# Kernel optimization log

Hardware: AMD Instinct MI355X
Metric: run time of the kernel (lower is better)

Reference implementation:

```python
import jax, jax.numpy as jnp
import numpy as np

B, C, H = 8, 768, 12
TH = TW = 16
SH = SW = 32
N = TH * TW + SH * SW  # 1280


def setup_inputs() -> dict:
    key = jax.random.key(0)
    k1, k2, k3 = jax.random.split(key, 3)
    return {
        "x": jax.random.normal(k1, (B, N, C), jnp.float32),
        "qkv_w": jax.random.normal(k2, (3 * C, C), jnp.float32) * 0.02,
        "proj_w": jax.random.normal(k3, (C, C), jnp.float32) * 0.02,
        "proj_b": jnp.zeros((C,), jnp.float32),
        "t_h": TH, "t_w": TW, "s_h": SH, "s_w": SW,
    }


def reference(x, qkv_w, proj_w, proj_b, t_h, t_w, s_h, s_w):
    Bb, Nn, Cc = x.shape
    hd = Cc // H
    scale = hd ** -0.5
    nt = t_h * t_w
    ns = s_h * s_w
    # qkv projection: torch Linear computes x @ W.T
    qkv = (x @ qkv_w.T).reshape(Bb, Nn, 3, H, hd).transpose(2, 0, 3, 1, 4)
    q, k, v = qkv[0], qkv[1], qkv[2]  # each [B, H, N, hd]
    q_mt, q_s = q[:, :, :nt], q[:, :, nt:]
    k_mt, v_mt = k[:, :, :nt], v[:, :, :nt]
    # template queries attend only to template keys
    attn_t = jax.nn.softmax(jnp.einsum('bhqd,bhkd->bhqk', q_mt, k_mt) * scale, axis=-1)
    x_mt = jnp.einsum('bhqk,bhkd->bhqd', attn_t, v_mt).transpose(0, 2, 1, 3).reshape(Bb, nt, Cc)
    # search queries attend to all (template + search) keys
    attn_s = jax.nn.softmax(jnp.einsum('bhqd,bhkd->bhqk', q_s, k) * scale, axis=-1)
    x_s = jnp.einsum('bhqk,bhkd->bhqd', attn_s, v).transpose(0, 2, 1, 3).reshape(Bb, ns, Cc)
    out = jnp.concatenate([x_mt, x_s], axis=1)
    out = out @ proj_w.T + proj_b
    return out
```

## Files before the change

### kernel.cpp

```cpp
#include <hip/hip_runtime.h>
#include <hip/hip_bf16.h>


typedef __attribute__((ext_vector_type(8))) short s8v;
typedef __attribute__((ext_vector_type(4))) float f4v;
typedef __attribute__((ext_vector_type(4))) unsigned short u4v;
typedef __attribute__((ext_vector_type(4))) unsigned int u4i;

#define MFMA16(a, b, c) __builtin_amdgcn_mfma_f32_16x16x32_bf16((a), (b), (c), 0, 0, 0)

#define QSCALE 0.1803368801f

__device__ __forceinline__ unsigned short f2bf(float f) {
  unsigned int u = __builtin_bit_cast(unsigned int, f);
  u += 0x7fffu + ((u >> 16) & 1u);
  return (unsigned short)(u >> 16);
}

__device__ __forceinline__ unsigned int pk2(float lo, float hi) {
  __hip_bfloat162 t = __float22bfloat162_rn(make_float2(lo, hi));
  unsigned int u;
  __builtin_memcpy(&u, &t, 4);
  return u;
}

__device__ __forceinline__ s8v pack8(const float* p0, const float* p1) {
  u4i pi;
  pi[0] = pk2(p0[0], p0[1]);
  pi[1] = pk2(p0[2], p0[3]);
  pi[2] = pk2(p1[0], p1[1]);
  pi[3] = pk2(p1[2], p1[3]);
  return __builtin_bit_cast(s8v, pi);
}

__global__ __launch_bounds__(256) void cvt3_kernel(const float* __restrict__ x,
                                                   const float* __restrict__ wq,
                                                   const float* __restrict__ wp,
                                                   unsigned short* __restrict__ xb,
                                                   unsigned short* __restrict__ wqb,
                                                   unsigned short* __restrict__ wpb) {
  int i = blockIdx.x * 256 + threadIdx.x;
  const float* src;
  unsigned short* dst;
  int j;
  if (i < 1966080) {
    src = x; dst = xb; j = i;
  } else if (i < 1966080 + 442368) {
    src = wq; dst = wqb; j = i - 1966080;
  } else {
    src = wp; dst = wpb; j = i - (1966080 + 442368);
  }
  f4v v = ((const f4v*)src)[j];
  u4v o;
  o[0] = f2bf(v[0]); o[1] = f2bf(v[1]); o[2] = f2bf(v[2]); o[3] = f2bf(v[3]);
  ((u4v*)dst)[j] = o;
}

__global__ __launch_bounds__(256) void gemm_qkv_kernel(
    const unsigned short* __restrict__ A,
    const unsigned short* __restrict__ Bm,
    unsigned short* __restrict__ qb, unsigned short* __restrict__ kb,
    unsigned short* __restrict__ vT) {
  const int K = 768;
  __shared__ __align__(16) unsigned short As[128 * 32];
  __shared__ __align__(16) unsigned short Bs[128 * 32];
  int tid = threadIdx.x;
  int wave = tid >> 6, lane = tid & 63;
  int quad = lane >> 4, l16 = lane & 15;
  int wm = wave >> 1, wn = wave & 1;
  int m0 = blockIdx.y * 128, n0 = blockIdx.x * 128;

  f4v acc[4][4];
#pragma unroll
  for (int i = 0; i < 4; ++i)
#pragma unroll
    for (int j = 0; j < 4; ++j) acc[i][j] = (f4v){0.f, 0.f, 0.f, 0.f};

  for (int kt = 0; kt < K; kt += 32) {
#pragma unroll
    for (int c = 0; c < 2; ++c) {
      int idx = c * 256 + tid;
      int row = idx >> 2;
      int col = (idx & 3) << 3;
      const unsigned short* ga = A + (size_t)(m0 + row) * K + (kt + col);
      const unsigned short* gb = Bm + (size_t)(n0 + row) * K + (kt + col);
      __builtin_amdgcn_global_load_lds(
          (const __attribute__((address_space(1))) unsigned int*)ga,
          (__attribute__((address_space(3))) unsigned int*)((char*)As + idx * 16), 16, 0, 0);
      __builtin_amdgcn_global_load_lds(
          (const __attribute__((address_space(1))) unsigned int*)gb,
          (__attribute__((address_space(3))) unsigned int*)((char*)Bs + idx * 16), 16, 0, 0);
    }
    __syncthreads();
    s8v af[4], bfr[4];
#pragma unroll
    for (int mi = 0; mi < 4; ++mi)
      af[mi] = *(const s8v*)&As[(wm * 64 + mi * 16 + l16) * 32 + quad * 8];
#pragma unroll
    for (int ni = 0; ni < 4; ++ni)
      bfr[ni] = *(const s8v*)&Bs[(wn * 64 + ni * 16 + l16) * 32 + quad * 8];
#pragma unroll
    for (int mi = 0; mi < 4; ++mi)
#pragma unroll
      for (int ni = 0; ni < 4; ++ni)
        acc[mi][ni] = MFMA16(af[mi], bfr[ni], acc[mi][ni]);
    __syncthreads();
  }

#pragma unroll
  for (int ni = 0; ni < 4; ++ni) {
    int gn = n0 + wn * 64 + ni * 16 + l16;
    int which = gn / 768;
    int oo = gn - which * 768;
    int hh = oo >> 6;
    int dd = oo & 63;
#pragma unroll
    for (int mi = 0; mi < 4; ++mi) {
#pragma unroll
      for (int r = 0; r < 4; ++r) {
        int gm = m0 + wm * 64 + mi * 16 + quad * 4 + r;
        int bb = gm / 1280;
        int nn = gm - bb * 1280;
        float v = acc[mi][ni][r];
        if (which == 0) {
          qb[(((size_t)bb * 12 + hh) * 1280 + nn) * 64 + dd] = f2bf(v * QSCALE);
        } else if (which == 1) {
          kb[(((size_t)bb * 12 + hh) * 1280 + nn) * 64 + dd] = f2bf(v);
        } else {
          vT[(((size_t)bb * 12 + hh) * 64 + dd) * 1280 + nn] = f2bf(v);
        }
      }
    }
  }
}

__global__ __launch_bounds__(256) void gemm_proj_kernel(
    const unsigned short* __restrict__ A,
    const unsigned short* __restrict__ Bm,
    const float* __restrict__ pb, float* __restrict__ out) {
  const int K = 768;
  __shared__ __align__(16) unsigned short As[128 * 32];
  __shared__ __align__(16) unsigned short Bs[128 * 32];
  int tid = threadIdx.x;
  int wave = tid >> 6, lane = tid & 63;
  int quad = lane >> 4, l16 = lane & 15;
  int wm = wave >> 1, wn = wave & 1;
  int m0 = blockIdx.y * 128, n0 = blockIdx.x * 128;

  f4v acc[4][4];
#pragma unroll
  for (int i = 0; i < 4; ++i)
#pragma unroll
    for (int j = 0; j < 4; ++j) acc[i][j] = (f4v){0.f, 0.f, 0.f, 0.f};

  for (int kt = 0; kt < K; kt += 32) {
#pragma unroll
    for (int c = 0; c < 2; ++c) {
      int idx = c * 256 + tid;
      int row = idx >> 2;
      int col = (idx & 3) << 3;
      const unsigned short* ga = A + (size_t)(m0 + row) * K + (kt + col);
      const unsigned short* gb = Bm + (size_t)(n0 + row) * K + (kt + col);
      __builtin_amdgcn_global_load_lds(
          (const __attribute__((address_space(1))) unsigned int*)ga,
          (__attribute__((address_space(3))) unsigned int*)((char*)As + idx * 16), 16, 0, 0);
      __builtin_amdgcn_global_load_lds(
          (const __attribute__((address_space(1))) unsigned int*)gb,
          (__attribute__((address_space(3))) unsigned int*)((char*)Bs + idx * 16), 16, 0, 0);
    }
    __syncthreads();
    s8v af[4], bfr[4];
#pragma unroll
    for (int mi = 0; mi < 4; ++mi)
      af[mi] = *(const s8v*)&As[(wm * 64 + mi * 16 + l16) * 32 + quad * 8];
#pragma unroll
    for (int ni = 0; ni < 4; ++ni)
      bfr[ni] = *(const s8v*)&Bs[(wn * 64 + ni * 16 + l16) * 32 + quad * 8];
#pragma unroll
    for (int mi = 0; mi < 4; ++mi)
#pragma unroll
      for (int ni = 0; ni < 4; ++ni)
        acc[mi][ni] = MFMA16(af[mi], bfr[ni], acc[mi][ni]);
    __syncthreads();
  }

#pragma unroll
  for (int ni = 0; ni < 4; ++ni) {
    int gn = n0 + wn * 64 + ni * 16 + l16;
    float bias = pb[gn];
#pragma unroll
    for (int mi = 0; mi < 4; ++mi)
#pragma unroll
      for (int r = 0; r < 4; ++r) {
        int gm = m0 + wm * 64 + mi * 16 + quad * 4 + r;
        out[(size_t)gm * 768 + gn] = acc[mi][ni][r] + bias;
      }
  }
}

__global__ __launch_bounds__(256) void attn_kernel(
    const unsigned short* __restrict__ qb, const unsigned short* __restrict__ kb,
    const unsigned short* __restrict__ vT, unsigned short* __restrict__ attnb) {
  const int NT = 1280, CC = 768;
  int bx = blockIdx.x;
  int h = blockIdx.y;
  int b = blockIdx.z;
  int nk, qstart;
  if (bx < 8) { nk = 1280; qstart = 256 + bx * 128; }
  else        { nk = 256;  qstart = (bx - 8) * 128; }
  int wave = threadIdx.x >> 6, lane = threadIdx.x & 63;
  int quad = lane >> 4, l16 = lane & 15;
  int qa = qstart + wave * 32;
  int ntiles = nk >> 6;

  const unsigned short* qp = qb + (((size_t)b * 12 + h) * NT + qa) * 64;
  const unsigned short* kp = kb + (((size_t)b * 12 + h) * NT) * 64;
  const unsigned short* vp = vT + (((size_t)b * 12 + h) * 64) * NT;

  __shared__ __align__(16) unsigned short Kl[2][8][512];
  __shared__ __align__(16) unsigned short Vl[2][8][512];

  s8v bq0 = *(const s8v*)(qp + l16 * 64 + quad * 8);
  s8v bq1 = *(const s8v*)(qp + l16 * 64 + 32 + quad * 8);
  s8v bq2 = *(const s8v*)(qp + (16 + l16) * 64 + quad * 8);
  s8v bq3 = *(const s8v*)(qp + (16 + l16) * 64 + 32 + quad * 8);

  int perm = ((l16 >> 2) << 3) + (l16 & 3);
  int f0 = wave * 2, f1 = wave * 2 + 1;
  int koffs0, koffs1, voffs0, voffs1;
  {
    int s = f0 >> 2, dh = (f0 >> 1) & 1, hh = f0 & 1;
    koffs0 = (s * 32 + hh * 4 + perm) * 64 + (dh * 4 + quad) * 8;
    s = f1 >> 2; dh = (f1 >> 1) & 1; hh = f1 & 1;
    koffs1 = (s * 32 + hh * 4 + perm) * 64 + (dh * 4 + quad) * 8;
    int dt = f0 >> 1, sv = f0 & 1;
    voffs0 = (dt * 16 + l16) * NT + sv * 32 + quad * 8;
    dt = f1 >> 1; sv = f1 & 1;
    voffs1 = (dt * 16 + l16) * NT + sv * 32 + quad * 8;
  }

#define STAGE(bfi, k0_)                                                                     \
  do {                                                                                      \
    __builtin_amdgcn_global_load_lds(                                                       \
        (const __attribute__((address_space(1))) unsigned int*)(kp + (size_t)(k0_)*64 +     \
                                                                koffs0),                    \
        (__attribute__((address_space(3))) unsigned int*)((char*)&Kl[bfi][f0][0] +          \
                                                          lane * 16),                       \
        16, 0, 0);                                                                          \
    __builtin_amdgcn_global_load_lds(                                                       \
        (const __attribute__((address_space(1))) unsigned int*)(kp + (size_t)(k0_)*64 +     \
                                                                koffs1),                    \
        (__attribute__((address_space(3))) unsigned int*)((char*)&Kl[bfi][f1][0] +          \
                                                          lane * 16),                       \
        16, 0, 0);                                                                          \
    __builtin_amdgcn_global_load_lds(                                                       \
        (const __attribute__((address_space(1))) unsigned int*)(vp + (size_t)(k0_) +        \
                                                                voffs0),                    \
        (__attribute__((address_space(3))) unsigned int*)((char*)&Vl[bfi][f0][0] +          \
                                                          lane * 16),                       \
        16, 0, 0);                                                                          \
    __builtin_amdgcn_global_load_lds(                                                       \
        (const __attribute__((address_space(1))) unsigned int*)(vp + (size_t)(k0_) +        \
                                                                voffs1),                    \
        (__attribute__((address_space(3))) unsigned int*)((char*)&Vl[bfi][f1][0] +          \
                                                          lane * 16),                       \
        16, 0, 0);                                                                          \
  } while (0)

  float la = 0.f, lb = 0.f;
  f4v Oa[4], Ob[4];
#pragma unroll
  for (int dt = 0; dt < 4; ++dt) {
    Oa[dt] = (f4v){0.f, 0.f, 0.f, 0.f};
    Ob[dt] = (f4v){0.f, 0.f, 0.f, 0.f};
  }

  STAGE(0, 0);

  for (int t = 0; t < ntiles; ++t) {
    __syncthreads();
    int bf = t & 1;
    if (t + 1 < ntiles) STAGE(bf ^ 1, (t + 1) * 64);

    s8v kf[8], vf[8];
#pragma unroll
    for (int f = 0; f < 8; ++f) kf[f] = *(const s8v*)&Kl[bf][f][lane * 8];
#pragma unroll
    for (int g = 0; g < 8; ++g) vf[g] = *(const s8v*)&Vl[bf][g][lane * 8];

#pragma unroll
    for (int s = 0; s < 2; ++s) {
      int s4 = s << 2;
      f4v s0a = {0.f, 0.f, 0.f, 0.f}, s1a = {0.f, 0.f, 0.f, 0.f};
      f4v s0b = {0.f, 0.f, 0.f, 0.f}, s1b = {0.f, 0.f, 0.f, 0.f};
      s0a = MFMA16(kf[s4 | 0], bq0, s0a);
      s0a = MFMA16(kf[s4 | 2], bq1, s0a);
      s1a = MFMA16(kf[s4 | 1], bq0, s1a);
      s1a = MFMA16(kf[s4 | 3], bq1, s1a);
      s0b = MFMA16(kf[s4 | 0], bq2, s0b);
      s0b = MFMA16(kf[s4 | 2], bq3, s0b);
      s1b = MFMA16(kf[s4 | 1], bq2, s1b);
      s1b = MFMA16(kf[s4 | 3], bq3, s1b);

      float p0a[4], p1a[4], p0b[4], p1b[4];
#pragma unroll
      for (int r = 0; r < 4; ++r) {
        p0a[r] = __builtin_amdgcn_exp2f(s0a[r]);
        p1a[r] = __builtin_amdgcn_exp2f(s1a[r]);
        p0b[r] = __builtin_amdgcn_exp2f(s0b[r]);
        p1b[r] = __builtin_amdgcn_exp2f(s1b[r]);
      }
      la += ((p0a[0] + p0a[1]) + (p0a[2] + p0a[3])) + ((p1a[0] + p1a[1]) + (p1a[2] + p1a[3]));
      lb += ((p0b[0] + p0b[1]) + (p0b[2] + p0b[3])) + ((p1b[0] + p1b[1]) + (p1b[2] + p1b[3]));

      s8v pa = pack8(p0a, p1a);
      s8v pbv = pack8(p0b, p1b);

#pragma unroll
      for (int dt = 0; dt < 4; ++dt) {
        Oa[dt] = MFMA16(vf[dt * 2 + s], pa, Oa[dt]);
        Ob[dt] = MFMA16(vf[dt * 2 + s], pbv, Ob[dt]);
      }
    }
  }
#undef STAGE

  la += __shfl_xor(la, 16, 64);
  la += __shfl_xor(la, 32, 64);
  lb += __shfl_xor(lb, 16, 64);
  lb += __shfl_xor(lb, 32, 64);
  float inva = 1.f / la, invb = 1.f / lb;

  size_t rowa = ((size_t)b * NT + qa + l16) * CC + h * 64;
  size_t rowb = ((size_t)b * NT + qa + 16 + l16) * CC + h * 64;
#pragma unroll
  for (int dt = 0; dt < 4; ++dt) {
    u4v ova, ovb;
#pragma unroll
    for (int r = 0; r < 4; ++r) {
      ova[r] = f2bf(Oa[dt][r] * inva);
      ovb[r] = f2bf(Ob[dt][r] * invb);
    }
    *(u4v*)(attnb + rowa + dt * 16 + quad * 4) = ova;
    *(u4v*)(attnb + rowb + dt * 16 + quad * 4) = ovb;
  }
}

extern "C" void kernel_launch(void* const* d_in, const int* in_sizes, int n_in,
                              void* d_out, int out_size, void* d_ws, size_t ws_size,
                              hipStream_t stream) {
  const float* x = (const float*)d_in[0];
  const float* qkv_w = (const float*)d_in[1];
  const float* proj_w = (const float*)d_in[2];
  const float* proj_b = (const float*)d_in[3];
  float* out = (float*)d_out;

  char* ws = (char*)d_ws;
  unsigned short* xb = (unsigned short*)(ws + 0);
  unsigned short* wqkvb = (unsigned short*)(ws + 15728640);
  unsigned short* wpb = (unsigned short*)(ws + 19267584);
  unsigned short* qb = (unsigned short*)(ws + 20447232);
  unsigned short* kbuf = (unsigned short*)(ws + 36175872);
  unsigned short* vT = (unsigned short*)(ws + 51904512);
  unsigned short* attnb = xb;

  cvt3_kernel<<<dim3(9984), 256, 0, stream>>>(x, qkv_w, proj_w, xb, wqkvb, wpb);

  gemm_qkv_kernel<<<dim3(18, 80), 256, 0, stream>>>(xb, wqkvb, qb, kbuf, vT);
  attn_kernel<<<dim3(10, 12, 8), 256, 0, stream>>>(qb, kbuf, vT, attnb);
  gemm_proj_kernel<<<dim3(6, 80), 256, 0, stream>>>(attnb, wpb, proj_b, out);
}
```

Baseline: 280.0 us.

## Double-buffer LDS tiles in QKV and projection GEMMs and vectorize V-transpose stores

Both GEMM kernels now use two LDS buffers, issuing the global-to-LDS loads for the next k-tile before computing on the current one, with one barrier per iteration instead of two. Global source pointers are precomputed outside the loop. The QKV epilogue is specialized per block, since n0 fixes whether a block writes q, k or v, and the transposed V output is written as packed 4-element bf16 stores instead of scalar stores. This doubles LDS use per block, which may reduce occupancy. The single barrier relies on the async LDS loads for the next buffer being ordered after all reads of that buffer from the previous iteration.

```diff
diff --git a/kernel.cpp b/kernel.cpp
--- a/kernel.cpp
+++ b/kernel.cpp
@@ -6,6 +6,7 @@
 typedef __attribute__((ext_vector_type(4))) float f4v;
 typedef __attribute__((ext_vector_type(4))) unsigned short u4v;
 typedef __attribute__((ext_vector_type(4))) unsigned int u4i;
+typedef __attribute__((ext_vector_type(2))) unsigned int u2i;
 
 #define MFMA16(a, b, c) __builtin_amdgcn_mfma_f32_16x16x32_bf16((a), (b), (c), 0, 0, 0)
 
@@ -56,78 +57,108 @@
   ((u4v*)dst)[j] = o;
 }
 
+
+#define GEMM_STAGE(AS, BS, kt_)                                                             \
+  do {                                                                                      \
+    __builtin_amdgcn_global_load_lds(                                                       \
+        (const __attribute__((address_space(1))) unsigned int*)(gA0 + (kt_)),               \
+        (__attribute__((address_space(3))) unsigned int*)((char*)(AS) + tid * 16), 16, 0, 0); \
+    __builtin_amdgcn_global_load_lds(                                                       \
+        (const __attribute__((address_space(1))) unsigned int*)(gB0 + (kt_)),               \
+        (__attribute__((address_space(3))) unsigned int*)((char*)(BS) + tid * 16), 16, 0, 0); \
+    __builtin_amdgcn_global_load_lds(                                                       \
+        (const __attribute__((address_space(1))) unsigned int*)(gA1 + (kt_)),               \
+        (__attribute__((address_space(3))) unsigned int*)((char*)(AS) + (256 + tid) * 16),  \
+        16, 0, 0);                                                                          \
+    __builtin_amdgcn_global_load_lds(                                                       \
+        (const __attribute__((address_space(1))) unsigned int*)(gB1 + (kt_)),               \
+        (__attribute__((address_space(3))) unsigned int*)((char*)(BS) + (256 + tid) * 16),  \
+        16, 0, 0);                                                                          \
+  } while (0)
+
 __global__ __launch_bounds__(256) void gemm_qkv_kernel(
     const unsigned short* __restrict__ A,
     const unsigned short* __restrict__ Bm,
     unsigned short* __restrict__ qb, unsigned short* __restrict__ kb,
     unsigned short* __restrict__ vT) {
   const int K = 768;
-  __shared__ __align__(16) unsigned short As[128 * 32];
-  __shared__ __align__(16) unsigned short Bs[128 * 32];
+  __shared__ __align__(16) unsigned short As[2][128 * 32];
+  __shared__ __align__(16) unsigned short Bs[2][128 * 32];
   int tid = threadIdx.x;
   int wave = tid >> 6, lane = tid & 63;
   int quad = lane >> 4, l16 = lane & 15;
   int wm = wave >> 1, wn = wave & 1;
   int m0 = blockIdx.y * 128, n0 = blockIdx.x * 128;
 
+  int srow = tid >> 2, scol = (tid & 3) << 3;
+  const unsigned short* gA0 = A + (size_t)(m0 + srow) * K + scol;
+  const unsigned short* gA1 = A + (size_t)(m0 + srow + 64) * K + scol;
+  const unsigned short* gB0 = Bm + (size_t)(n0 + srow) * K + scol;
+  const unsigned short* gB1 = Bm + (size_t)(n0 + srow + 64) * K + scol;
+
   f4v acc[4][4];
 #pragma unroll
   for (int i = 0; i < 4; ++i)
 #pragma unroll
     for (int j = 0; j < 4; ++j) acc[i][j] = (f4v){0.f, 0.f, 0.f, 0.f};
 
-  for (int kt = 0; kt < K; kt += 32) {
-#pragma unroll
-    for (int c = 0; c < 2; ++c) {
-      int idx = c * 256 + tid;
-      int row = idx >> 2;
-      int col = (idx & 3) << 3;
-      const unsigned short* ga = A + (size_t)(m0 + row) * K + (kt + col);
-      const unsigned short* gb = Bm + (size_t)(n0 + row) * K + (kt + col);
-      __builtin_amdgcn_global_load_lds(
-          (const __attribute__((address_space(1))) unsigned int*)ga,
-          (__attribute__((address_space(3))) unsigned int*)((char*)As + idx * 16), 16, 0, 0);
-      __builtin_amdgcn_global_load_lds(
-          (const __attribute__((address_space(1))) unsigned int*)gb,
-          (__attribute__((address_space(3))) unsigned int*)((char*)Bs + idx * 16), 16, 0, 0);
-    }
+  GEMM_STAGE(As[0], Bs[0], 0);
+
+  for (int t = 0; t < 24; ++t) {
     __syncthreads();
+    int bf = t & 1;
+    if (t + 1 < 24) GEMM_STAGE(As[bf ^ 1], Bs[bf ^ 1], (t + 1) * 32);
+
+    const unsigned short* Ab = As[bf];
+    const unsigned short* Bb = Bs[bf];
     s8v af[4], bfr[4];
 #pragma unroll
     for (int mi = 0; mi < 4; ++mi)
-      af[mi] = *(const s8v*)&As[(wm * 64 + mi * 16 + l16) * 32 + quad * 8];
+      af[mi] = *(const s8v*)&Ab[(wm * 64 + mi * 16 + l16) * 32 + quad * 8];
 #pragma unroll
     for (int ni = 0; ni < 4; ++ni)
-      bfr[ni] = *(const s8v*)&Bs[(wn * 64 + ni * 16 + l16) * 32 + quad * 8];
+      bfr[ni] = *(const s8v*)&Bb[(wn * 64 + ni * 16 + l16) * 32 + quad * 8];
 #pragma unroll
     for (int mi = 0; mi < 4; ++mi)
 #pragma unroll
       for (int ni = 0; ni < 4; ++ni)
         acc[mi][ni] = MFMA16(af[mi], bfr[ni], acc[mi][ni]);
-    __syncthreads();
-  }
-
-#pragma unroll
-  for (int ni = 0; ni < 4; ++ni) {
-    int gn = n0 + wn * 64 + ni * 16 + l16;
-    int which = gn / 768;
-    int oo = gn - which * 768;
-    int hh = oo >> 6;
-    int dd = oo & 63;
-#pragma unroll
-    for (int mi = 0; mi < 4; ++mi) {
-#pragma unroll
-      for (int r = 0; r < 4; ++r) {
-        int gm = m0 + wm * 64 + mi * 16 + quad * 4 + r;
+  }
+
+  int which = n0 / 768;
+  if (which == 2) {
+#pragma unroll
+    for (int ni = 0; ni < 4; ++ni) {
+      int oo = n0 + wn * 64 + ni * 16 + l16 - 1536;
+      int hh = oo >> 6;
+      int dd = oo & 63;
+#pragma unroll
+      for (int mi = 0; mi < 4; ++mi) {
+        int gm = m0 + wm * 64 + mi * 16 + quad * 4;
         int bb = gm / 1280;
         int nn = gm - bb * 1280;
-        float v = acc[mi][ni][r];
-        if (which == 0) {
-          qb[(((size_t)bb * 12 + hh) * 1280 + nn) * 64 + dd] = f2bf(v * QSCALE);
-        } else if (which == 1) {
-          kb[(((size_t)bb * 12 + hh) * 1280 + nn) * 64 + dd] = f2bf(v);
-        } else {
-          vT[(((size_t)bb * 12 + hh) * 64 + dd) * 1280 + nn] = f2bf(v);
+        u2i w;
+        w[0] = pk2(acc[mi][ni][0], acc[mi][ni][1]);
+        w[1] = pk2(acc[mi][ni][2], acc[mi][ni][3]);
+        *(u2i*)(vT + (((size_t)bb * 12 + hh) * 64 + dd) * 1280 + nn) = w;
+      }
+    }
+  } else {
+    unsigned short* dst = which ? kb : qb;
+    float sc = which ? 1.0f : QSCALE;
+#pragma unroll
+    for (int ni = 0; ni < 4; ++ni) {
+      int oo = n0 + wn * 64 + ni * 16 + l16 - which * 768;
+      int hh = oo >> 6;
+      int dd = oo & 63;
+#pragma unroll
+      for (int mi = 0; mi < 4; ++mi) {
+#pragma unroll
+        for (int r = 0; r < 4; ++r) {
+          int gm = m0 + wm * 64 + mi * 16 + quad * 4 + r;
+          int bb = gm / 1280;
+          int nn = gm - bb * 1280;
+          dst[(((size_t)bb * 12 + hh) * 1280 + nn) * 64 + dd] = f2bf(acc[mi][ni][r] * sc);
         }
       }
     }
@@ -139,49 +170,47 @@
     const unsigned short* __restrict__ Bm,
     const float* __restrict__ pb, float* __restrict__ out) {
   const int K = 768;
-  __shared__ __align__(16) unsigned short As[128 * 32];
-  __shared__ __align__(16) unsigned short Bs[128 * 32];
+  __shared__ __align__(16) unsigned short As[2][128 * 32];
+  __shared__ __align__(16) unsigned short Bs[2][128 * 32];
   int tid = threadIdx.x;
   int wave = tid >> 6, lane = tid & 63;
   int quad = lane >> 4, l16 = lane & 15;
   int wm = wave >> 1, wn = wave & 1;
   int m0 = blockIdx.y * 128, n0 = blockIdx.x * 128;
 
+  int srow = tid >> 2, scol = (tid & 3) << 3;
+  const unsigned short* gA0 = A + (size_t)(m0 + srow) * K + scol;
+  const unsigned short* gA1 = A + (size_t)(m0 + srow + 64) * K + scol;
+  const unsigned short* gB0 = Bm + (size_t)(n0 + srow) * K + scol;
+  const unsigned short* gB1 = Bm + (size_t)(n0 + srow + 64) * K + scol;
+
   f4v acc[4][4];
 #pragma unroll
   for (int i = 0; i < 4; ++i)
 #pragma unroll
     for (int j = 0; j < 4; ++j) acc[i][j] = (f4v){0.f, 0.f, 0.f, 0.f};
 
-  for (int kt = 0; kt < K; kt += 32) {
-#pragma unroll
-    for (int c = 0; c < 2; ++c) {
-      int idx = c * 256 + tid;
-      int row = idx >> 2;
-      int col = (idx & 3) << 3;
-      const unsigned short* ga = A + (size_t)(m0 + row) * K + (kt + col);
-      const unsigned short* gb = Bm + (size_t)(n0 + row) * K + (kt + col);
-      __builtin_amdgcn_global_load_lds(
-          (const __attribute__((address_space(1))) unsigned int*)ga,
-          (__attribute__((address_space(3))) unsigned int*)((char*)As + idx * 16), 16, 0, 0);
-      __builtin_amdgcn_global_load_lds(
-          (const __attribute__((address_space(1))) unsigned int*)gb,
-          (__attribute__((address_space(3))) unsigned int*)((char*)Bs + idx * 16), 16, 0, 0);
-    }
+  GEMM_STAGE(As[0], Bs[0], 0);
+
+  for (int t = 0; t < 24; ++t) {
     __syncthreads();
+    int bf = t & 1;
+    if (t + 1 < 24) GEMM_STAGE(As[bf ^ 1], Bs[bf ^ 1], (t + 1) * 32);
+
+    const unsigned short* Ab = As[bf];
+    const unsigned short* Bb = Bs[bf];
     s8v af[4], bfr[4];
 #pragma unroll
     for (int mi = 0; mi < 4; ++mi)
-      af[mi] = *(const s8v*)&As[(wm * 64 + mi * 16 + l16) * 32 + quad * 8];
+      af[mi] = *(const s8v*)&Ab[(wm * 64 + mi * 16 + l16) * 32 + quad * 8];
 #pragma unroll
     for (int ni = 0; ni < 4; ++ni)
-      bfr[ni] = *(const s8v*)&Bs[(wn * 64 + ni * 16 + l16) * 32 + quad * 8];
+      bfr[ni] = *(const s8v*)&Bb[(wn * 64 + ni * 16 + l16) * 32 + quad * 8];
 #pragma unroll
     for (int mi = 0; mi < 4; ++mi)
 #pragma unroll
       for (int ni = 0; ni < 4; ++ni)
         acc[mi][ni] = MFMA16(af[mi], bfr[ni], acc[mi][ni]);
-    __syncthreads();
   }
 
 #pragma unroll
```

After: 272.0 us. 2.9% less time.
